# Kernel optimization log

Measured on AMD Instinct MI355X. Metric: run time of the kernel, lower is better.

The kernel has to match this reference:

```python
import jax, jax.numpy as jnp
import numpy as np


def setup_inputs() -> dict:
    key = jax.random.key(0)
    k1, k2 = jax.random.split(key)
    B, C, T = 16, 256, 1500
    K = 2048
    x = jax.random.normal(k1, (B, C, T), dtype=jnp.float32)
    # torch init: uniform(-1/K, 1/K)
    codebook = jax.random.uniform(k2, (K, C), dtype=jnp.float32,
                                  minval=-1.0 / K, maxval=1.0 / K)
    return {"x": x, "codebook": codebook}


def reference(x, codebook):
    B, C, T = x.shape
    # (B, T, C) -> (B*T, C)
    x_flat = jnp.transpose(x, (0, 2, 1)).reshape(-1, C)
    distances = (jnp.sum(x_flat * x_flat, axis=1, keepdims=True)
                 - 2.0 * x_flat @ codebook.T
                 + jnp.sum(codebook * codebook, axis=1))  # (B*T, K)
    indices = jnp.argmin(distances, axis=1)               # (B*T,)
    quantized_flat = codebook[indices]                    # (B*T, C)
    quantized = jnp.transpose(quantized_flat.reshape(B, T, C), (0, 2, 1))
    indices_out = indices.reshape(B, 1, T)
    # straight-through estimator
    quantized_out = x + jax.lax.stop_gradient(quantized - x)
    commitment_loss = jnp.mean((jax.lax.stop_gradient(quantized) - x) ** 2)
    return quantized_out, indices_out, commitment_loss
```

## Files before the change

### kernel.cpp

```cpp
#include <hip/hip_runtime.h>
#include <stdint.h>


#define B_DIM 16
#define C_DIM 256
#define T_DIM 1500
#define K_CODES 2048
#define N_ROWS (B_DIM * T_DIM)
#define TOTAL_ELEMS (B_DIM * C_DIM * T_DIM)

#define TM 64
#define TKC 256
#define CS 32
#define KSLICE 512
#define OT 64

__device__ __forceinline__ void gl_lds16(const float* g, float* l) {
    __builtin_amdgcn_global_load_lds(
        (const __attribute__((address_space(1))) void*)(uintptr_t)g,
        (__attribute__((address_space(3))) void*)(uintptr_t)l, 16, 0, 0);
}

__global__ __launch_bounds__(256) void vq_transpose(const float* __restrict__ x,
                                                    float* __restrict__ xT) {
    __shared__ float tile[32][33];
    const int b = blockIdx.z;
    const int t0 = blockIdx.x * 32;
    const int c0 = blockIdx.y * 32;
    const int tx = threadIdx.x & 31;
    const int ty = threadIdx.x >> 5;
#pragma unroll
    for (int q = 0; q < 4; ++q) {
        const int c = c0 + ty * 4 + q;
        int t = t0 + tx; if (t >= T_DIM) t = T_DIM - 1;
        tile[ty * 4 + q][tx] = x[((size_t)b * C_DIM + c) * T_DIM + t];
    }
    __syncthreads();
#pragma unroll
    for (int q = 0; q < 4; ++q) {
        const int t = t0 + ty * 4 + q;
        if (t < T_DIM)
            xT[((size_t)b * T_DIM + t) * C_DIM + c0 + tx] = tile[tx][ty * 4 + q];
    }
}

__global__ __launch_bounds__(256) void vq_se(const float* __restrict__ cb,
                                             float* __restrict__ Se) {
    const int k = blockIdx.x * 256 + threadIdx.x;
    if (k >= K_CODES) return;
    const float* row = cb + (size_t)k * C_DIM;
    float h[2];
#pragma unroll
    for (int half = 0; half < 2; ++half) {
        const float* a = row + half * 128;
        float r[8];
#pragma unroll
        for (int j = 0; j < 8; ++j) r[j] = __fmul_rn(a[j], a[j]);
        for (int i = 8; i < 128; i += 8)
#pragma unroll
            for (int j = 0; j < 8; ++j)
                r[j] = __fadd_rn(r[j], __fmul_rn(a[i + j], a[i + j]));
        h[half] = __fadd_rn(
            __fadd_rn(__fadd_rn(r[0], r[1]), __fadd_rn(r[2], r[3])),
            __fadd_rn(__fadd_rn(r[4], r[5]), __fadd_rn(r[6], r[7])));
    }
    Se[k] = __fadd_rn(h[0], h[1]);
}

__global__ __launch_bounds__(256) void vq_sx(const float* __restrict__ xT,
                                             float* __restrict__ Sx) {
    const int n = blockIdx.x * 256 + threadIdx.x;
    if (n >= N_ROWS) return;
    const float* row = xT + (size_t)n * C_DIM;
    float h[2];
#pragma unroll
    for (int half = 0; half < 2; ++half) {
        const float* a = row + half * 128;
        float r[8];
#pragma unroll
        for (int j = 0; j < 8; ++j) r[j] = __fmul_rn(a[j], a[j]);
        for (int i = 8; i < 128; i += 8)
#pragma unroll
            for (int j = 0; j < 8; ++j)
                r[j] = __fadd_rn(r[j], __fmul_rn(a[i + j], a[i + j]));
        h[half] = __fadd_rn(
            __fadd_rn(__fadd_rn(r[0], r[1]), __fadd_rn(r[2], r[3])),
            __fadd_rn(__fadd_rn(r[4], r[5]), __fadd_rn(r[6], r[7])));
    }
    Sx[n] = __fadd_rn(h[0], h[1]);
}

__global__ void vq_init(unsigned long long* __restrict__ slots) {
    const int n = blockIdx.x * 256 + threadIdx.x;
    if (n < N_ROWS) slots[n] = ~0ull;
}

__global__ __launch_bounds__(256) void vq_argmin(
    const float* __restrict__ xT, const float* __restrict__ cb,
    const float* __restrict__ Se, const float* __restrict__ Sx,
    unsigned long long* __restrict__ slots) {
    __shared__ float xs[TM * CS];
    __shared__ float cs[TKC * CS];
    __shared__ float e2s[TKC];
    __shared__ float Sxs[TM];

    const int tid = threadIdx.x;
    const int t0 = blockIdx.x * TM;
    const int b = blockIdx.y;
    const int k0 = blockIdx.z * KSLICE;
    const int tr = tid & 7;
    const int tcol = tid >> 3;

    if (tid < TM) {
        int t = t0 + tid;
        Sxs[tid] = (t < T_DIM) ? Sx[b * T_DIM + t] : 0.f;
    }

    float m1[8];
    int k1[8];
#pragma unroll
    for (int i = 0; i < 8; ++i) { m1[i] = 1e30f; k1[i] = 0x7fffffff; }

    const float* xTb = xT + (size_t)b * T_DIM * C_DIM;

    for (int kc = 0; kc < KSLICE; kc += TKC) {
        __syncthreads();
        e2s[tid] = Se[k0 + kc + tid];

        float acc[8][8];
#pragma unroll
        for (int i = 0; i < 8; ++i)
#pragma unroll
            for (int j = 0; j < 8; ++j) acc[i][j] = 0.f;

        for (int c0 = 0; c0 < C_DIM; c0 += CS) {
            __syncthreads();
#pragma unroll
            for (int p = 0; p < 2; ++p) {
                const int A = p * 256 + tid;
                const int r = A >> 3, slot = A & 7;
                const int g4 = slot ^ ((r >> 3) & 7);
                int t = t0 + r; if (t >= T_DIM) t = T_DIM - 1;
                gl_lds16(xTb + (size_t)t * C_DIM + c0 + g4 * 4, &xs[A * 4]);
            }
#pragma unroll
            for (int i = 0; i < 8; ++i) {
                const int A = i * 256 + tid;
                const int kk = A >> 3, slot = A & 7;
                const int g4 = slot ^ ((kk >> 3) & 7);
                gl_lds16(cb + (size_t)(k0 + kc + kk) * C_DIM + c0 + g4 * 4,
                         &cs[A * 4]);
            }
            __syncthreads();
#pragma unroll
            for (int g = 0; g < 8; ++g) {
                float4 cv[8];
#pragma unroll
                for (int j = 0; j < 8; ++j)
                    cv[j] = *reinterpret_cast<const float4*>(
                        &cs[(tcol * 8 + j) * CS + ((g ^ (tcol & 7)) << 2)]);
#pragma unroll
                for (int i = 0; i < 8; ++i) {
                    const float4 xv = *reinterpret_cast<const float4*>(
                        &xs[(tr * 8 + i) * CS + ((g ^ tr) << 2)]);
#pragma unroll
                    for (int j = 0; j < 8; ++j) {
                        acc[i][j] = fmaf(xv.x, cv[j].x, acc[i][j]);
                        acc[i][j] = fmaf(xv.y, cv[j].y, acc[i][j]);
                        acc[i][j] = fmaf(xv.z, cv[j].z, acc[i][j]);
                        acc[i][j] = fmaf(xv.w, cv[j].w, acc[i][j]);
                    }
                }
            }
        }
#pragma unroll
        for (int j = 0; j < 8; ++j) {
            const float ev = e2s[tcol * 8 + j];
            const int kg = k0 + kc + tcol * 8 + j;
#pragma unroll
            for (int i = 0; i < 8; ++i) {
                const float s = __fadd_rn(
                    __fsub_rn(Sxs[tr * 8 + i], __fmul_rn(2.0f, acc[i][j])), ev);
                if (s < m1[i]) { m1[i] = s; k1[i] = kg; }
            }
        }
    }

    __syncthreads();
    float* redm = cs;
    int* redk = reinterpret_cast<int*>(cs + TM * 32);
#pragma unroll
    for (int i = 0; i < 8; ++i) {
        const int r = tr * 8 + i;
        redm[r * 32 + tcol] = m1[i];
        redk[r * 32 + tcol] = k1[i];
    }
    __syncthreads();
    if (tid < TM) {
        const int r = tid;
        float bm = 1e30f;
        int bk = 0x7fffffff;
        for (int tc = 0; tc < 32; ++tc) {
            const float c1 = redm[r * 32 + tc];
            const int ck = redk[r * 32 + tc];
            if (c1 < bm || (c1 == bm && ck < bk)) { bm = c1; bk = ck; }
        }
        const int t = t0 + r;
        if (t < T_DIM) {
            const unsigned long long pack =
                ((unsigned long long)__float_as_uint(bm) << 32) | (unsigned)bk;
            atomicMin(slots + b * T_DIM + t, pack);
        }
    }
}

__global__ __launch_bounds__(256) void vq_output(
    const float* __restrict__ x, const float* __restrict__ cb,
    const unsigned long long* __restrict__ slots, float* __restrict__ out,
    float* __restrict__ partials) {
    const int tid = threadIdx.x;
    const int b = blockIdx.y;
    const int t0 = blockIdx.x * OT;
    __shared__ int idxs[OT];
    if (tid < OT) {
        const int t = t0 + tid;
        if (t < T_DIM) {
            const int id = (int)(unsigned)(slots[b * T_DIM + t] & 0xffffffffull);
            idxs[tid] = id;
            out[(size_t)TOTAL_ELEMS + b * T_DIM + t] = (float)id;
        }
    }
    __syncthreads();
    const int ti = tid & 63;
    const int cq = tid >> 6;
    const int t = t0 + ti;
    float lsum = 0.f;
    if (t < T_DIM) {
        const int id = idxs[ti];
        for (int c0 = 0; c0 < C_DIM; c0 += 4) {
            const int c = c0 + cq;
            const size_t off = (size_t)(b * C_DIM + c) * T_DIM + t;
            const float xv = x[off];
            const float q = cb[(size_t)id * C_DIM + c];
            out[off] = __fadd_rn(xv, __fsub_rn(q, xv));
            const float d = __fsub_rn(q, xv);
            lsum = fmaf(d, d, lsum);
        }
    }
#pragma unroll
    for (int off = 32; off; off >>= 1) lsum += __shfl_down(lsum, off, 64);
    __shared__ float wsum[4];
    if ((tid & 63) == 0) wsum[tid >> 6] = lsum;
    __syncthreads();
    if (tid == 0)
        partials[blockIdx.y * gridDim.x + blockIdx.x] =
            wsum[0] + wsum[1] + wsum[2] + wsum[3];
}

__global__ void vq_loss(const float* __restrict__ partials, int nparts,
                        float* __restrict__ out) {
    __shared__ float red[256];
    float s = 0.f;
    for (int i = threadIdx.x; i < nparts; i += 256) s += partials[i];
    red[threadIdx.x] = s;
    __syncthreads();
    for (int off = 128; off; off >>= 1) {
        if (threadIdx.x < off) red[threadIdx.x] += red[threadIdx.x + off];
        __syncthreads();
    }
    if (threadIdx.x == 0)
        out[(size_t)TOTAL_ELEMS + N_ROWS] = red[0] * (1.0f / (float)TOTAL_ELEMS);
}

extern "C" void kernel_launch(void* const* d_in, const int* in_sizes, int n_in,
                              void* d_out, int out_size, void* d_ws, size_t ws_size,
                              hipStream_t stream) {
    const float* x = (const float*)d_in[0];
    const float* cb = (const float*)d_in[1];
    float* out = (float*)d_out;

    float* xT = out;

    float* Se = (float*)d_ws;
    float* Sx = Se + K_CODES;
    unsigned long long* slots =
        (unsigned long long*)((char*)d_ws + ((8192 + 96000 + 7) & ~7ull));
    float* partials = (float*)(slots + N_ROWS);

    vq_transpose<<<dim3(47, 8, B_DIM), dim3(256), 0, stream>>>(x, xT);
    vq_se<<<dim3(K_CODES / 256), dim3(256), 0, stream>>>(cb, Se);
    vq_sx<<<dim3((N_ROWS + 255) / 256), dim3(256), 0, stream>>>(xT, Sx);
    vq_init<<<dim3((N_ROWS + 255) / 256), dim3(256), 0, stream>>>(slots);
    vq_argmin<<<dim3((T_DIM + TM - 1) / TM, B_DIM, K_CODES / KSLICE),
                dim3(256), 0, stream>>>(xT, cb, Se, Sx, slots);
    vq_output<<<dim3((T_DIM + OT - 1) / OT, B_DIM), dim3(256), 0, stream>>>(
        x, cb, slots, out, partials);
    vq_loss<<<dim3(1), dim3(256), 0, stream>>>(
        partials, (T_DIM + OT - 1) / OT * B_DIM, out);
}
```

Measured before the change: 387.2 us.

## Drop LDS staging in argmin GEMM; load operands directly from global memory

Removes the global-to-LDS async staging and the per-chunk barriers from the distance kernel. Each thread now reads its x rows and codebook rows straight from global memory (through the cache) as float4 loads. KSLICE is halved so each block covers 256 codes in a single pass, which doubles the grid in the K dimension and adds more atomicMin traffic. The aim is to cut synchronization and LDS overhead. The risk is that the new loads are strided, uncoalesced and served from L1/L2, which may starve the FMA loop.

```diff
diff --git a/kernel.cpp b/kernel.cpp
--- a/kernel.cpp
+++ b/kernel.cpp
@@ -10,16 +10,8 @@
 #define TOTAL_ELEMS (B_DIM * C_DIM * T_DIM)
 
 #define TM 64
-#define TKC 256
-#define CS 32
-#define KSLICE 512
+#define KSLICE 256
 #define OT 64
-
-__device__ __forceinline__ void gl_lds16(const float* g, float* l) {
-    __builtin_amdgcn_global_load_lds(
-        (const __attribute__((address_space(1))) void*)(uintptr_t)g,
-        (__attribute__((address_space(3))) void*)(uintptr_t)l, 16, 0, 0);
-}
 
 __global__ __launch_bounds__(256) void vq_transpose(const float* __restrict__ x,
                                                     float* __restrict__ xT) {
@@ -99,101 +91,88 @@
     const float* __restrict__ xT, const float* __restrict__ cb,
     const float* __restrict__ Se, const float* __restrict__ Sx,
     unsigned long long* __restrict__ slots) {
-    __shared__ float xs[TM * CS];
-    __shared__ float cs[TKC * CS];
-    __shared__ float e2s[TKC];
-    __shared__ float Sxs[TM];
+    __shared__ float redm[32 * 64];
+    __shared__ int   redk[32 * 64];
 
     const int tid = threadIdx.x;
     const int t0 = blockIdx.x * TM;
     const int b = blockIdx.y;
-    const int k0 = blockIdx.z * KSLICE;
+    const int k0 = blockIdx.z * KSLICE + (tid >> 3) * 8;
     const int tr = tid & 7;
     const int tcol = tid >> 3;
 
-    if (tid < TM) {
-        int t = t0 + tid;
-        Sxs[tid] = (t < T_DIM) ? Sx[b * T_DIM + t] : 0.f;
-    }
-
+    const float* xr[8];
+#pragma unroll
+    for (int i = 0; i < 8; ++i) {
+        int t = t0 + tr * 8 + i;
+        if (t >= T_DIM) t = T_DIM - 1;
+        xr[i] = xT + ((size_t)b * T_DIM + t) * C_DIM;
+    }
+    const float* cb0 = cb + (size_t)k0 * C_DIM;
+    const float* cb4 = cb0 + 4 * C_DIM;
+
+    float acc[8][8];
+#pragma unroll
+    for (int i = 0; i < 8; ++i)
+#pragma unroll
+        for (int j = 0; j < 8; ++j) acc[i][j] = 0.f;
+
+#pragma unroll 2
+    for (int g = 0; g < 64; ++g) {
+        float4 cv[8];
+#pragma unroll
+        for (int j4 = 0; j4 < 4; ++j4) {
+            cv[j4]     = *reinterpret_cast<const float4*>(cb0 + (size_t)j4 * C_DIM + g * 4);
+            cv[j4 + 4] = *reinterpret_cast<const float4*>(cb4 + (size_t)j4 * C_DIM + g * 4);
+        }
+#pragma unroll
+        for (int ih = 0; ih < 2; ++ih) {
+            float4 xv[4];
+#pragma unroll
+            for (int ii = 0; ii < 4; ++ii)
+                xv[ii] = *reinterpret_cast<const float4*>(xr[ih * 4 + ii] + g * 4);
+#pragma unroll
+            for (int ii = 0; ii < 4; ++ii) {
+                const int i = ih * 4 + ii;
+#pragma unroll
+                for (int j = 0; j < 8; ++j) {
+                    acc[i][j] = fmaf(xv[ii].x, cv[j].x, acc[i][j]);
+                    acc[i][j] = fmaf(xv[ii].y, cv[j].y, acc[i][j]);
+                    acc[i][j] = fmaf(xv[ii].z, cv[j].z, acc[i][j]);
+                    acc[i][j] = fmaf(xv[ii].w, cv[j].w, acc[i][j]);
+                }
+            }
+        }
+    }
+
+    float sxr[8];
+#pragma unroll
+    for (int i = 0; i < 8; ++i) {
+        int t = t0 + tr * 8 + i;
+        if (t >= T_DIM) t = T_DIM - 1;
+        sxr[i] = Sx[b * T_DIM + t];
+    }
     float m1[8];
     int k1[8];
 #pragma unroll
     for (int i = 0; i < 8; ++i) { m1[i] = 1e30f; k1[i] = 0x7fffffff; }
-
-    const float* xTb = xT + (size_t)b * T_DIM * C_DIM;
-
-    for (int kc = 0; kc < KSLICE; kc += TKC) {
-        __syncthreads();
-        e2s[tid] = Se[k0 + kc + tid];
-
-        float acc[8][8];
-#pragma unroll
-        for (int i = 0; i < 8; ++i)
-#pragma unroll
-            for (int j = 0; j < 8; ++j) acc[i][j] = 0.f;
-
-        for (int c0 = 0; c0 < C_DIM; c0 += CS) {
-            __syncthreads();
-#pragma unroll
-            for (int p = 0; p < 2; ++p) {
-                const int A = p * 256 + tid;
-                const int r = A >> 3, slot = A & 7;
-                const int g4 = slot ^ ((r >> 3) & 7);
-                int t = t0 + r; if (t >= T_DIM) t = T_DIM - 1;
-                gl_lds16(xTb + (size_t)t * C_DIM + c0 + g4 * 4, &xs[A * 4]);
-            }
-#pragma unroll
-            for (int i = 0; i < 8; ++i) {
-                const int A = i * 256 + tid;
-                const int kk = A >> 3, slot = A & 7;
-                const int g4 = slot ^ ((kk >> 3) & 7);
-                gl_lds16(cb + (size_t)(k0 + kc + kk) * C_DIM + c0 + g4 * 4,
-                         &cs[A * 4]);
-            }
-            __syncthreads();
-#pragma unroll
-            for (int g = 0; g < 8; ++g) {
-                float4 cv[8];
-#pragma unroll
-                for (int j = 0; j < 8; ++j)
-                    cv[j] = *reinterpret_cast<const float4*>(
-                        &cs[(tcol * 8 + j) * CS + ((g ^ (tcol & 7)) << 2)]);
-#pragma unroll
-                for (int i = 0; i < 8; ++i) {
-                    const float4 xv = *reinterpret_cast<const float4*>(
-                        &xs[(tr * 8 + i) * CS + ((g ^ tr) << 2)]);
-#pragma unroll
-                    for (int j = 0; j < 8; ++j) {
-                        acc[i][j] = fmaf(xv.x, cv[j].x, acc[i][j]);
-                        acc[i][j] = fmaf(xv.y, cv[j].y, acc[i][j]);
-                        acc[i][j] = fmaf(xv.z, cv[j].z, acc[i][j]);
-                        acc[i][j] = fmaf(xv.w, cv[j].w, acc[i][j]);
-                    }
-                }
-            }
-        }
-#pragma unroll
-        for (int j = 0; j < 8; ++j) {
-            const float ev = e2s[tcol * 8 + j];
-            const int kg = k0 + kc + tcol * 8 + j;
-#pragma unroll
-            for (int i = 0; i < 8; ++i) {
-                const float s = __fadd_rn(
-                    __fsub_rn(Sxs[tr * 8 + i], __fmul_rn(2.0f, acc[i][j])), ev);
-                if (s < m1[i]) { m1[i] = s; k1[i] = kg; }
-            }
-        }
-    }
-
-    __syncthreads();
-    float* redm = cs;
-    int* redk = reinterpret_cast<int*>(cs + TM * 32);
+#pragma unroll
+    for (int j = 0; j < 8; ++j) {
+        const float ev = Se[k0 + j];
+        const int kg = k0 + j;
+#pragma unroll
+        for (int i = 0; i < 8; ++i) {
+            const float s = __fadd_rn(
+                __fsub_rn(sxr[i], __fmul_rn(2.0f, acc[i][j])), ev);
+            if (s < m1[i]) { m1[i] = s; k1[i] = kg; }
+        }
+    }
+
 #pragma unroll
     for (int i = 0; i < 8; ++i) {
         const int r = tr * 8 + i;
-        redm[r * 32 + tcol] = m1[i];
-        redk[r * 32 + tcol] = k1[i];
+        redm[tcol * 64 + r] = m1[i];
+        redk[tcol * 64 + r] = k1[i];
     }
     __syncthreads();
     if (tid < TM) {
@@ -201,8 +180,8 @@
         float bm = 1e30f;
         int bk = 0x7fffffff;
         for (int tc = 0; tc < 32; ++tc) {
-            const float c1 = redm[r * 32 + tc];
-            const int ck = redk[r * 32 + tc];
+            const float c1 = redm[tc * 64 + r];
+            const int ck = redk[tc * 64 + r];
             if (c1 < bm || (c1 == bm && ck < bk)) { bm = c1; bk = ck; }
         }
         const int t = t0 + r;
```

After: 911.7 us. 135% more time.

## Read x tile straight from global, shrink code slice, raise occupancy in argmin

Applied to the files above, without the earlier changes.

The argmin kernel no longer stages the x tile in LDS. Each thread loads its eight x rows straight from global memory inside the inner product loop, and LDS holds only the codebook tile. Each block now covers a single 256-code slice, so the grid has twice as many blocks along K, and the squared-norm terms are loaded into registers at the end. A launch-bounds occupancy hint of 4 is added and the reduction scratch layout is transposed. The aim is to cut LDS traffic and barriers and raise parallelism, but the redundant global x loads depend on cache hits, and register pressure under the occupancy cap risks spills.

```diff
diff --git a/kernel.cpp b/kernel.cpp
--- a/kernel.cpp
+++ b/kernel.cpp
@@ -12,7 +12,6 @@
 #define TM 64
 #define TKC 256
 #define CS 32
-#define KSLICE 512
 #define OT 64
 
 __device__ __forceinline__ void gl_lds16(const float* g, float* l) {
@@ -95,74 +94,54 @@
     if (n < N_ROWS) slots[n] = ~0ull;
 }
 
-__global__ __launch_bounds__(256) void vq_argmin(
+__global__ __launch_bounds__(256, 4) void vq_argmin(
     const float* __restrict__ xT, const float* __restrict__ cb,
     const float* __restrict__ Se, const float* __restrict__ Sx,
     unsigned long long* __restrict__ slots) {
-    __shared__ float xs[TM * CS];
     __shared__ float cs[TKC * CS];
-    __shared__ float e2s[TKC];
-    __shared__ float Sxs[TM];
 
     const int tid = threadIdx.x;
     const int t0 = blockIdx.x * TM;
     const int b = blockIdx.y;
-    const int k0 = blockIdx.z * KSLICE;
+    const int k0 = blockIdx.z * TKC;
     const int tr = tid & 7;
     const int tcol = tid >> 3;
 
-    if (tid < TM) {
-        int t = t0 + tid;
-        Sxs[tid] = (t < T_DIM) ? Sx[b * T_DIM + t] : 0.f;
-    }
-
-    float m1[8];
-    int k1[8];
-#pragma unroll
-    for (int i = 0; i < 8; ++i) { m1[i] = 1e30f; k1[i] = 0x7fffffff; }
-
-    const float* xTb = xT + (size_t)b * T_DIM * C_DIM;
-
-    for (int kc = 0; kc < KSLICE; kc += TKC) {
+    const float* xb0 = xT + ((size_t)b * T_DIM + t0 + tr * 8) * C_DIM;
+    const float* xb4 = xb0 + 4 * C_DIM;
+
+    float acc[8][8];
+#pragma unroll
+    for (int i = 0; i < 8; ++i)
+#pragma unroll
+        for (int j = 0; j < 8; ++j) acc[i][j] = 0.f;
+
+#pragma unroll 1
+    for (int c0 = 0; c0 < C_DIM; c0 += CS) {
         __syncthreads();
-        e2s[tid] = Se[k0 + kc + tid];
-
-        float acc[8][8];
-#pragma unroll
-        for (int i = 0; i < 8; ++i)
-#pragma unroll
-            for (int j = 0; j < 8; ++j) acc[i][j] = 0.f;
-
-        for (int c0 = 0; c0 < C_DIM; c0 += CS) {
-            __syncthreads();
-#pragma unroll
-            for (int p = 0; p < 2; ++p) {
-                const int A = p * 256 + tid;
-                const int r = A >> 3, slot = A & 7;
-                const int g4 = slot ^ ((r >> 3) & 7);
-                int t = t0 + r; if (t >= T_DIM) t = T_DIM - 1;
-                gl_lds16(xTb + (size_t)t * C_DIM + c0 + g4 * 4, &xs[A * 4]);
-            }
-#pragma unroll
-            for (int i = 0; i < 8; ++i) {
-                const int A = i * 256 + tid;
-                const int kk = A >> 3, slot = A & 7;
-                const int g4 = slot ^ ((kk >> 3) & 7);
-                gl_lds16(cb + (size_t)(k0 + kc + kk) * C_DIM + c0 + g4 * 4,
-                         &cs[A * 4]);
-            }
-            __syncthreads();
-#pragma unroll
-            for (int g = 0; g < 8; ++g) {
-                float4 cv[8];
-#pragma unroll
-                for (int j = 0; j < 8; ++j)
-                    cv[j] = *reinterpret_cast<const float4*>(
-                        &cs[(tcol * 8 + j) * CS + ((g ^ (tcol & 7)) << 2)]);
-#pragma unroll
-                for (int i = 0; i < 8; ++i) {
+#pragma unroll
+        for (int i = 0; i < 8; ++i) {
+            const int A = i * 256 + tid;
+            const int kk = A >> 3, slot = A & 7;
+            const int g4 = slot ^ ((kk >> 3) & 7);
+            gl_lds16(cb + (size_t)(k0 + kk) * C_DIM + c0 + g4 * 4, &cs[A * 4]);
+        }
+        __syncthreads();
+#pragma unroll
+        for (int g = 0; g < 8; ++g) {
+            float4 cv[8];
+#pragma unroll
+            for (int j = 0; j < 8; ++j)
+                cv[j] = *reinterpret_cast<const float4*>(
+                    &cs[(tcol * 8 + j) * CS + ((g ^ (tcol & 7)) << 2)]);
+#pragma unroll
+            for (int ih = 0; ih < 2; ++ih) {
+                const float* xb = ih ? xb4 : xb0;
+#pragma unroll
+                for (int ii = 0; ii < 4; ++ii) {
+                    const int i = ih * 4 + ii;
                     const float4 xv = *reinterpret_cast<const float4*>(
-                        &xs[(tr * 8 + i) * CS + ((g ^ tr) << 2)]);
+                        xb + (size_t)ii * C_DIM + c0 + g * 4);
 #pragma unroll
                     for (int j = 0; j < 8; ++j) {
                         acc[i][j] = fmaf(xv.x, cv[j].x, acc[i][j]);
@@ -173,27 +152,43 @@
                 }
             }
         }
-#pragma unroll
-        for (int j = 0; j < 8; ++j) {
-            const float ev = e2s[tcol * 8 + j];
-            const int kg = k0 + kc + tcol * 8 + j;
-#pragma unroll
-            for (int i = 0; i < 8; ++i) {
-                const float s = __fadd_rn(
-                    __fsub_rn(Sxs[tr * 8 + i], __fmul_rn(2.0f, acc[i][j])), ev);
-                if (s < m1[i]) { m1[i] = s; k1[i] = kg; }
-            }
+    }
+
+    float sxr[8], evr[8];
+#pragma unroll
+    for (int i = 0; i < 8; ++i) {
+        int t = t0 + tr * 8 + i; if (t >= T_DIM) t = T_DIM - 1;
+        sxr[i] = Sx[b * T_DIM + t];
+    }
+    {
+        const float4 e0 = *reinterpret_cast<const float4*>(Se + k0 + tcol * 8);
+        const float4 e1 = *reinterpret_cast<const float4*>(Se + k0 + tcol * 8 + 4);
+        evr[0] = e0.x; evr[1] = e0.y; evr[2] = e0.z; evr[3] = e0.w;
+        evr[4] = e1.x; evr[5] = e1.y; evr[6] = e1.z; evr[7] = e1.w;
+    }
+    float m1[8];
+    int k1[8];
+#pragma unroll
+    for (int i = 0; i < 8; ++i) { m1[i] = 1e30f; k1[i] = 0x7fffffff; }
+#pragma unroll
+    for (int j = 0; j < 8; ++j) {
+        const int kg = k0 + tcol * 8 + j;
+#pragma unroll
+        for (int i = 0; i < 8; ++i) {
+            const float s = __fadd_rn(
+                __fsub_rn(sxr[i], __fmul_rn(2.0f, acc[i][j])), evr[j]);
+            if (s < m1[i]) { m1[i] = s; k1[i] = kg; }
         }
     }
 
     __syncthreads();
     float* redm = cs;
-    int* redk = reinterpret_cast<int*>(cs + TM * 32);
+    int* redk = reinterpret_cast<int*>(cs + 32 * 64);
 #pragma unroll
     for (int i = 0; i < 8; ++i) {
         const int r = tr * 8 + i;
-        redm[r * 32 + tcol] = m1[i];
-        redk[r * 32 + tcol] = k1[i];
+        redm[tcol * 64 + r] = m1[i];
+        redk[tcol * 64 + r] = k1[i];
     }
     __syncthreads();
     if (tid < TM) {
@@ -201,8 +196,8 @@
         float bm = 1e30f;
         int bk = 0x7fffffff;
         for (int tc = 0; tc < 32; ++tc) {
-            const float c1 = redm[r * 32 + tc];
-            const int ck = redk[r * 32 + tc];
+            const float c1 = redm[tc * 64 + r];
+            const int ck = redk[tc * 64 + r];
             if (c1 < bm || (c1 == bm && ck < bk)) { bm = c1; bk = ck; }
         }
         const int t = t0 + r;
@@ -291,7 +286,7 @@
     vq_se<<<dim3(K_CODES / 256), dim3(256), 0, stream>>>(cb, Se);
     vq_sx<<<dim3((N_ROWS + 255) / 256), dim3(256), 0, stream>>>(xT, Sx);
     vq_init<<<dim3((N_ROWS + 255) / 256), dim3(256), 0, stream>>>(slots);
-    vq_argmin<<<dim3((T_DIM + TM - 1) / TM, B_DIM, K_CODES / KSLICE),
+    vq_argmin<<<dim3((T_DIM + TM - 1) / TM, B_DIM, K_CODES / TKC),
                 dim3(256), 0, stream>>>(xT, cb, Se, Sx, slots);
     vq_output<<<dim3((T_DIM + OT - 1) / OT, B_DIM), dim3(256), 0, stream>>>(
         x, cb, slots, out, partials);
```

Result: slower. 976.4 us (+152.2%).
